# Optimization experiments

Measured on AMD Instinct MI355X. Metric: run time of the kernel, lower is better.

## Reference

```python
import jax, jax.numpy as jnp
import numpy as np

H, W, C = 56, 56, 384
WS, SHIFT, HEADS = 7, 3, 12
HEAD_DIM = C // HEADS
SCALE = HEAD_DIM ** (-0.5)
NWIN = (H // WS) * (W // WS)  # 64 windows per image
NTOK = WS * WS                # 49 tokens per window
EPS = 1e-5


def _gen_mask():
    # static shift-window attention mask, computed with numpy (jit-safe constant)
    img = np.zeros((H, W))
    sl = (slice(0, -WS), slice(-WS, -SHIFT), slice(-SHIFT, None))
    cnt = 0
    for hs in sl:
        for ws in sl:
            img[hs, ws] = cnt
            cnt += 1
    mw = img.reshape(H // WS, WS, W // WS, WS).transpose(0, 2, 1, 3).reshape(-1, NTOK)
    diff = mw[:, None, :] - mw[:, :, None]  # (NWIN, NTOK, NTOK)
    return jnp.asarray(np.where(diff != 0, -100.0, 0.0), dtype=jnp.float32)

ATTN_MASK = _gen_mask()


def _layernorm(x, g, b):
    mu = jnp.mean(x, axis=-1, keepdims=True)
    var = jnp.var(x, axis=-1, keepdims=True)
    return (x - mu) * jax.lax.rsqrt(var + EPS) * g + b


def setup_inputs() -> dict:
    key = jax.random.key(0)
    ks = jax.random.split(key, 6)
    s = 0.02
    return {
        "x": jax.random.normal(ks[0], (16, H * W, C), dtype=jnp.float32),
        "ln1_g": jnp.ones((C,), jnp.float32),
        "ln1_b": jnp.zeros((C,), jnp.float32),
        "qkv_w": jax.random.normal(ks[1], (C, 3 * C), jnp.float32) * s,
        "proj_w": jax.random.normal(ks[2], (C, C), jnp.float32) * s,
        "proj_b": jnp.zeros((C,), jnp.float32),
        "ln2_g": jnp.ones((C,), jnp.float32),
        "ln2_b": jnp.zeros((C,), jnp.float32),
        "fc1_w": jax.random.normal(ks[3], (C, 4 * C), jnp.float32) * s,
        "fc1_b": jnp.zeros((4 * C,), jnp.float32),
        "fc2_w": jax.random.normal(ks[4], (4 * C, C), jnp.float32) * s,
        "fc2_b": jnp.zeros((C,), jnp.float32),
    }


def reference(x, ln1_g, ln1_b, qkv_w, proj_w, proj_b, ln2_g, ln2_b, fc1_w, fc1_b, fc2_w, fc2_b):
    B, N, _ = x.shape
    h = x
    y = _layernorm(x, ln1_g, ln1_b).reshape(B, H, W, C)
    # cyclic shift (note: source never rolls back; we match it)
    y = jnp.roll(y, shift=(-SHIFT, -SHIFT), axis=(1, 2))
    # window partition -> (B*NWIN, NTOK, C)
    y = y.reshape(B, H // WS, WS, W // WS, WS, C).transpose(0, 1, 3, 2, 4, 5)
    y = y.reshape(B * NWIN, NTOK, C)
    # qkv (no bias), split heads
    qkv = (y @ qkv_w).reshape(B * NWIN, NTOK, 3, HEADS, HEAD_DIM)
    qkv = qkv.transpose(2, 0, 3, 1, 4)  # (3, BW, heads, NTOK, hd)
    q, k, v = qkv[0], qkv[1], qkv[2]
    attn = jnp.einsum('whnd,whmd->whnm', q, k) * SCALE  # (BW, heads, NTOK, NTOK)
    attn = attn.reshape(B, NWIN, HEADS, NTOK, NTOK) + ATTN_MASK[None, :, None]
    attn = jax.nn.softmax(attn.reshape(B * NWIN, HEADS, NTOK, NTOK), axis=-1)
    o = jnp.einsum('whnm,whmd->whnd', attn, v)
    o = o.transpose(0, 2, 1, 3).reshape(B * NWIN, NTOK, C)
    o = o @ proj_w + proj_b
    # window reverse -> (B, N, C)
    o = o.reshape(B, H // WS, W // WS, WS, WS, C).transpose(0, 1, 3, 2, 4, 5)
    o = o.reshape(B, N, C)
    x1 = h + o
    # MLP (GELU after both fc1 and fc2, as in source)
    m = _layernorm(x1, ln2_g, ln2_b)
    m = jax.nn.gelu(m @ fc1_w + fc1_b, approximate=False)
    m = jax.nn.gelu(m @ fc2_w + fc2_b, approximate=False)
    return x1 + m
```

## Files before the change

kernel.cpp:

```cpp
#include <hip/hip_runtime.h>
#include <hip/hip_bf16.h>
#include <cstdint>
#include <cstddef>

#define C_DIM   384
#define NIMG    3136
#define MROWS   50176
#define QK_SCALE 0.17677669529663687f

using bf16x8 = __attribute__((ext_vector_type(8))) short;
using f32x4  = __attribute__((ext_vector_type(4))) float;

__device__ __forceinline__ short f2bf(float f) {
  union { float f; uint32_t u; } v; v.f = f;
  uint32_t r = (v.u + 0x7fffu + ((v.u >> 16) & 1u)) >> 16;
  return (short)(uint16_t)r;
}

__device__ __forceinline__ float bf2f(short s) {
  union { uint32_t u; float f; } v; v.u = ((uint32_t)(uint16_t)s) << 16;
  return v.f;
}

__device__ __forceinline__ void async_copy16(const void* g, void* l) {
  __builtin_amdgcn_global_load_lds(
      (const __attribute__((address_space(1))) void*)g,
      (__attribute__((address_space(3))) void*)l, 16, 0, 0);
}

__device__ __forceinline__ float gelu_exact(float x) {
  return 0.5f * x * (1.0f + erff(x * 0.7071067811865475f));
}

__global__ __launch_bounds__(256) void transpose_cast(
    const float* __restrict__ w, short* __restrict__ wt, int K, int N) {
  int idx = blockIdx.x * 256 + threadIdx.x;
  if (idx >= K * N) return;
  int k = idx / N;
  int n = idx - k * N;
  wt[(size_t)n * K + k] = f2bf(w[idx]);
}

template <typename IN>
__global__ __launch_bounds__(256) void ln_kernel(
    const IN* __restrict__ x, const float* __restrict__ g,
    const float* __restrict__ b, short* __restrict__ y, int windowed) {
  int token = blockIdx.x * 4 + (threadIdx.x >> 6);
  int lane = threadIdx.x & 63;
  size_t src;
  if (windowed) {
    int bw = token / 49;
    int tt = token - bw * 49;
    int bb = bw >> 6, w = bw & 63;
    int hs = (w >> 3) * 7 + tt / 7 + 3; if (hs >= 56) hs -= 56;
    int ws = (w & 7) * 7 + (tt % 7) + 3; if (ws >= 56) ws -= 56;
    src = (size_t)(bb * NIMG + hs * 56 + ws) * C_DIM;
  } else {
    src = (size_t)token * C_DIM;
  }
  const IN* xr = x + src;
  float v[6];
  float s = 0.f;
#pragma unroll
  for (int i = 0; i < 6; ++i) {
    if constexpr (sizeof(IN) == 4) v[i] = (float)xr[lane + i * 64];
    else v[i] = bf2f((short)xr[lane + i * 64]);
    s += v[i];
  }
#pragma unroll
  for (int m = 1; m < 64; m <<= 1) s += __shfl_xor(s, m);
  float mu = s * (1.0f / 384.0f);
  float var = 0.f;
#pragma unroll
  for (int i = 0; i < 6; ++i) { float d = v[i] - mu; var += d * d; }
#pragma unroll
  for (int m = 1; m < 64; m <<= 1) var += __shfl_xor(var, m);
  float rstd = rsqrtf(var * (1.0f / 384.0f) + 1e-5f);
  short* yr = y + (size_t)token * C_DIM;
#pragma unroll
  for (int i = 0; i < 6; ++i) {
    int c = lane + i * 64;
    yr[c] = f2bf((v[i] - mu) * rstd * g[c] + b[c]);
  }
}

template <int EPI>
__global__ __launch_bounds__(256, 2) void gemm_kernel(
    const short* __restrict__ A, const short* __restrict__ Bt,
    void* __restrict__ Out, const float* __restrict__ bias,
    const void* __restrict__ resid, int M, int N, int K, int nby) {
  __shared__ __align__(16) short lds[2][128 * 64 * 2];
  const int t = threadIdx.x;
  const int wave = t >> 6, lane = t & 63;
  const int lrow = lane & 15, quad = lane >> 4;
  const int wm = wave & 1, wn = wave >> 1;

  const int wg = (int)blockIdx.x;
  const int swz = (wg & 7) * ((int)gridDim.x >> 3) + (wg >> 3);
  const int mb = swz / nby;
  const int nb = swz - mb * nby;
  const int m0 = mb * 128, n0 = nb * 128;

  f32x4 acc[4][4] = {};

  const int srow = t >> 3;
  const int spos = t & 7;

  const int nt = K >> 6;

  auto stage = [&](int buf, int k0) {
    short* la = &lds[buf][0];
    short* lb = la + 128 * 64;
#pragma unroll
    for (int i = 0; i < 4; ++i) {
      int row = i * 32 + srow;
      int ca = spos ^ (row & 7);
      async_copy16(A + (size_t)(m0 + row) * K + k0 + ca * 8,
                   la + (i * 32 + wave * 8) * 64);
      async_copy16(Bt + (size_t)(n0 + row) * K + k0 + ca * 8,
                   lb + (i * 32 + wave * 8) * 64);
    }
  };

  stage(0, 0);

  for (int kt = 0; kt < nt; ++kt) {
    __builtin_amdgcn_sched_barrier(0);
    if (kt + 1 < nt) {
      stage((kt + 1) & 1, (kt + 1) * 64);
      asm volatile("s_waitcnt vmcnt(8)" ::: "memory");
    } else {
      asm volatile("s_waitcnt vmcnt(0)" ::: "memory");
    }
    __builtin_amdgcn_s_barrier();
    __builtin_amdgcn_sched_barrier(0);

    short* ldsA = &lds[kt & 1][0];
    short* ldsB = ldsA + 128 * 64;
#pragma unroll
    for (int ks = 0; ks < 2; ++ks) {
      const int cb = ks * 4;
      bf16x8 af[4], bfr[4];
#pragma unroll
      for (int i = 0; i < 4; ++i) {
        int ra = wm * 64 + i * 16 + lrow;
        af[i] = *(const bf16x8*)(ldsA + ra * 64 + (((cb + quad) ^ (ra & 7)) * 8));
        int rb = wn * 64 + i * 16 + lrow;
        bfr[i] = *(const bf16x8*)(ldsB + rb * 64 + (((cb + quad) ^ (rb & 7)) * 8));
      }
      __builtin_amdgcn_s_setprio(1);
#pragma unroll
      for (int i = 0; i < 4; ++i)
#pragma unroll
        for (int j = 0; j < 4; ++j)
          acc[i][j] = __builtin_amdgcn_mfma_f32_16x16x32_bf16(af[i], bfr[j],
                                                              acc[i][j], 0, 0, 0);
      __builtin_amdgcn_s_setprio(0);
    }
    __builtin_amdgcn_sched_barrier(0);
    __builtin_amdgcn_s_barrier();
  }

#pragma unroll
  for (int i = 0; i < 4; ++i) {
#pragma unroll
    for (int r = 0; r < 4; ++r) {
      int row = m0 + wm * 64 + i * 16 + quad * 4 + r;
      if (EPI == 1) {
        int bw = row / 49;
        int tt = row - bw * 49;
        int bb = bw >> 6, w = bw & 63;
        int nimg = ((w >> 3) * 7 + tt / 7) * 56 + (w & 7) * 7 + (tt % 7);
        size_t obase = ((size_t)(bb * NIMG + nimg)) * C_DIM;
#pragma unroll
        for (int j = 0; j < 4; ++j) {
          int col = n0 + wn * 64 + j * 16 + lrow;
          size_t oi = obase + col;
          ((short*)Out)[oi] =
              f2bf(acc[i][j][r] + bias[col] + ((const float*)resid)[oi]);
        }
      } else {
#pragma unroll
        for (int j = 0; j < 4; ++j) {
          int col = n0 + wn * 64 + j * 16 + lrow;
          float v = acc[i][j][r];
          if (EPI == 0) {
            ((short*)Out)[(size_t)row * N + col] = f2bf(v);
          } else if (EPI == 2) {
            ((short*)Out)[(size_t)row * N + col] = f2bf(gelu_exact(v + bias[col]));
          } else {
            size_t oi = (size_t)row * C_DIM + col;
            ((float*)Out)[oi] =
                bf2f(((const short*)resid)[oi]) + gelu_exact(v + bias[col]);
          }
        }
      }
    }
  }
}

__global__ __launch_bounds__(256) void attn_kernel(
    const short* __restrict__ qkv, short* __restrict__ o) {
  __shared__ __align__(16) short plds[4][64 * 72];
  const int wavei = threadIdx.x >> 6;
  const int lane = threadIdx.x & 63;
  const int gw = blockIdx.x * 4 + wavei;
  const int bw = gw / 12;
  const int h = gw - bw * 12;
  const int w = bw & 63;
  const int lrow = lane & 15, quad = lane >> 4;
  const short* base = qkv + (size_t)bw * 49 * 1152 + h * 32;

  bf16x8 qf[4], kf[4];
#pragma unroll
  for (int i = 0; i < 4; ++i) {
    int tq = i * 16 + lrow;
    const short* p = base + (size_t)tq * 1152 + quad * 8;
    qf[i] = *(const bf16x8*)p;
    kf[i] = *(const bf16x8*)(p + 384);
  }
  f32x4 sa[4][4] = {};
#pragma unroll
  for (int i = 0; i < 4; ++i)
#pragma unroll
    for (int j = 0; j < 4; ++j)
      sa[i][j] = __builtin_amdgcn_mfma_f32_16x16x32_bf16(qf[i], kf[j], sa[i][j], 0, 0, 0);

  int tl = lane < 49 ? lane : 0;
  int rr = tl / 7, cc = tl - rr * 7;
  int hs = (w >> 3) * 7 + rr;
  int ws = (w & 7) * 7 + cc;
  int id = (hs < 49 ? 0 : (hs < 53 ? 3 : 6)) + (ws < 49 ? 0 : (ws < 53 ? 1 : 2));

  int idn[4], idm[4][4];
#pragma unroll
  for (int j = 0; j < 4; ++j) idn[j] = __shfl(id, j * 16 + lrow);
#pragma unroll
  for (int i = 0; i < 4; ++i)
#pragma unroll
    for (int r = 0; r < 4; ++r) idm[i][r] = __shfl(id, i * 16 + quad * 4 + r);

#pragma unroll
  for (int i = 0; i < 4; ++i)
#pragma unroll
    for (int j = 0; j < 4; ++j)
#pragma unroll
      for (int r = 0; r < 4; ++r) {
        float v = sa[i][j][r] * QK_SCALE + (idm[i][r] == idn[j] ? 0.f : -100.f);
        sa[i][j][r] = (j * 16 + lrow < 49) ? v : -1e30f;
      }

#pragma unroll
  for (int i = 0; i < 4; ++i)
#pragma unroll
    for (int r = 0; r < 4; ++r) {
      float mx = -1e30f;
#pragma unroll
      for (int j = 0; j < 4; ++j) mx = fmaxf(mx, sa[i][j][r]);
#pragma unroll
      for (int m = 1; m < 16; m <<= 1) mx = fmaxf(mx, __shfl_xor(mx, m));
      float sum = 0.f;
#pragma unroll
      for (int j = 0; j < 4; ++j) {
        float e = exp2f((sa[i][j][r] - mx) * 1.44269504f);
        sa[i][j][r] = e;
        sum += e;
      }
#pragma unroll
      for (int m = 1; m < 16; m <<= 1) sum += __shfl_xor(sum, m);
      float inv = 1.0f / sum;
#pragma unroll
      for (int j = 0; j < 4; ++j) sa[i][j][r] *= inv;
    }

  short* pw = plds[wavei];
#pragma unroll
  for (int i = 0; i < 4; ++i)
#pragma unroll
    for (int r = 0; r < 4; ++r)
#pragma unroll
      for (int j = 0; j < 4; ++j)
        pw[(i * 16 + quad * 4 + r) * 72 + j * 16 + lrow] = f2bf(sa[i][j][r]);

  f32x4 oa[4][2] = {};
#pragma unroll
  for (int kk = 0; kk < 2; ++kk) {
    bf16x8 vf[2];
#pragma unroll
    for (int j2 = 0; j2 < 2; ++j2) {
#pragma unroll
      for (int jj = 0; jj < 8; ++jj) {
        int n = kk * 32 + quad * 8 + jj;
        vf[j2][jj] = (n < 49)
            ? base[768 + (size_t)n * 1152 + j2 * 16 + lrow]
            : (short)0;
      }
    }
#pragma unroll
    for (int i = 0; i < 4; ++i) {
      bf16x8 pf = *(const bf16x8*)(pw + (i * 16 + lrow) * 72 + kk * 32 + quad * 8);
#pragma unroll
      for (int j2 = 0; j2 < 2; ++j2)
        oa[i][j2] = __builtin_amdgcn_mfma_f32_16x16x32_bf16(pf, vf[j2], oa[i][j2], 0, 0, 0);
    }
  }

#pragma unroll
  for (int i = 0; i < 4; ++i)
#pragma unroll
    for (int j2 = 0; j2 < 2; ++j2)
#pragma unroll
      for (int r = 0; r < 4; ++r) {
        int m = i * 16 + quad * 4 + r;
        if (m < 49)
          o[((size_t)bw * 49 + m) * 384 + h * 32 + j2 * 16 + lrow] = f2bf(oa[i][j2][r]);
      }
}

extern "C" void kernel_launch(void* const* d_in, const int* in_sizes, int n_in,
                              void* d_out, int out_size, void* d_ws, size_t ws_size,
                              hipStream_t stream) {
  const float* x      = (const float*)d_in[0];
  const float* ln1_g  = (const float*)d_in[1];
  const float* ln1_b  = (const float*)d_in[2];
  const float* qkv_w  = (const float*)d_in[3];
  const float* proj_w = (const float*)d_in[4];
  const float* proj_b = (const float*)d_in[5];
  const float* ln2_g  = (const float*)d_in[6];
  const float* ln2_b  = (const float*)d_in[7];
  const float* fc1_w  = (const float*)d_in[8];
  const float* fc1_b  = (const float*)d_in[9];
  const float* fc2_w  = (const float*)d_in[10];
  const float* fc2_b  = (const float*)d_in[11];
  float* out = (float*)d_out;

  char* ws = (char*)d_ws;
  auto alloc = [&](size_t bytes) {
    char* p = ws;
    ws += (bytes + 255) & ~(size_t)255;
    return p;
  };
  short* qkv_wT  = (short*)alloc((size_t)1152 * 384 * 2);
  short* proj_wT = (short*)alloc((size_t)384 * 384 * 2);
  short* fc1_wT  = (short*)alloc((size_t)1536 * 384 * 2);
  short* fc2_wT  = (short*)alloc((size_t)384 * 1536 * 2);
  short* bufA    = (short*)alloc((size_t)MROWS * 384 * 2);
  short* x1      = (short*)alloc((size_t)MROWS * 384 * 2);
  short* bufB    = (short*)alloc((size_t)MROWS * 1536 * 2);

  transpose_cast<<<(384 * 1152) / 256, 256, 0, stream>>>(qkv_w, qkv_wT, 384, 1152);
  transpose_cast<<<(384 * 384) / 256, 256, 0, stream>>>(proj_w, proj_wT, 384, 384);
  transpose_cast<<<(384 * 1536) / 256, 256, 0, stream>>>(fc1_w, fc1_wT, 384, 1536);
  transpose_cast<<<(1536 * 384) / 256, 256, 0, stream>>>(fc2_w, fc2_wT, 1536, 384);

  ln_kernel<float><<<MROWS / 4, 256, 0, stream>>>(x, ln1_g, ln1_b, bufA, 1);

  gemm_kernel<0><<<392 * 9, 256, 0, stream>>>(bufA, qkv_wT, bufB, nullptr,
                                              nullptr, MROWS, 1152, 384, 9);

  attn_kernel<<<3072, 256, 0, stream>>>(bufB, bufA);

  gemm_kernel<1><<<392 * 3, 256, 0, stream>>>(bufA, proj_wT, x1, proj_b,
                                              x, MROWS, 384, 384, 3);

  ln_kernel<short><<<MROWS / 4, 256, 0, stream>>>(x1, ln2_g, ln2_b, bufA, 0);

  gemm_kernel<2><<<392 * 12, 256, 0, stream>>>(bufA, fc1_wT, bufB, fc1_b,
                                               nullptr, MROWS, 1536, 384, 12);

  gemm_kernel<3><<<392 * 3, 256, 0, stream>>>(bufB, fc2_wT, out, fc2_b,
                                              x1, MROWS, 384, 1536, 3);
}
```

Measured before the change: 572.7 us.

## Add single-buffer high-occupancy GEMM variant for short-K GEMMs and fast GELU

Adds a PIPE template parameter to the GEMM. The K=384 GEMMs (qkv, proj, fc1) now use a single LDS buffer with plain syncthreads staging and launch bounds allowing 4 blocks per CU. Only the K=1536 fc2 GEMM keeps the double-buffered pipeline. The erf-based GELU is also replaced by an Abramowitz-Stegun polynomial with a hardware reciprocal and exp2, which cuts epilogue cost but is slightly less accurate.

```diff
diff --git a/kernel.cpp b/kernel.cpp
--- a/kernel.cpp
+++ b/kernel.cpp
@@ -28,8 +28,15 @@
       (__attribute__((address_space(3))) void*)l, 16, 0, 0);
 }
 
-__device__ __forceinline__ float gelu_exact(float x) {
-  return 0.5f * x * (1.0f + erff(x * 0.7071067811865475f));
+__device__ __forceinline__ float gelu_fast(float x) {
+  float z = fabsf(x) * 0.7071067811865476f;
+  float t = __builtin_amdgcn_rcpf(fmaf(0.3275911f, z, 1.0f));
+  float p = t * fmaf(t, fmaf(t, fmaf(t, fmaf(t, 1.061405429f, -1.453152027f),
+                                     1.421413741f), -0.284496736f),
+                     0.254829592f);
+  float e = p * exp2f(z * z * -1.4426950408889634f);
+  float phi2 = (x >= 0.0f) ? (2.0f - e) : e;
+  return 0.5f * x * phi2;
 }
 
 __global__ __launch_bounds__(256) void transpose_cast(
@@ -84,12 +91,13 @@
   }
 }
 
-template <int EPI>
-__global__ __launch_bounds__(256, 2) void gemm_kernel(
+template <int EPI, int PIPE>
+__global__ __launch_bounds__(256, PIPE ? 2 : 4) void gemm_kernel(
     const short* __restrict__ A, const short* __restrict__ Bt,
     void* __restrict__ Out, const float* __restrict__ bias,
     const void* __restrict__ resid, int M, int N, int K, int nby) {
-  __shared__ __align__(16) short lds[2][128 * 64 * 2];
+  constexpr int NBUF = PIPE ? 2 : 1;
+  __shared__ __align__(16) short lds[NBUF][128 * 64 * 2];
   const int t = threadIdx.x;
   const int wave = t >> 6, lane = t & 63;
   const int lrow = lane & 15, quad = lane >> 4;
@@ -122,20 +130,8 @@
     }
   };
 
-  stage(0, 0);
-
-  for (int kt = 0; kt < nt; ++kt) {
-    __builtin_amdgcn_sched_barrier(0);
-    if (kt + 1 < nt) {
-      stage((kt + 1) & 1, (kt + 1) * 64);
-      asm volatile("s_waitcnt vmcnt(8)" ::: "memory");
-    } else {
-      asm volatile("s_waitcnt vmcnt(0)" ::: "memory");
-    }
-    __builtin_amdgcn_s_barrier();
-    __builtin_amdgcn_sched_barrier(0);
-
-    short* ldsA = &lds[kt & 1][0];
+  auto compute = [&](int buf) {
+    short* ldsA = &lds[buf][0];
     short* ldsB = ldsA + 128 * 64;
 #pragma unroll
     for (int ks = 0; ks < 2; ++ks) {
@@ -148,17 +144,40 @@
         int rb = wn * 64 + i * 16 + lrow;
         bfr[i] = *(const bf16x8*)(ldsB + rb * 64 + (((cb + quad) ^ (rb & 7)) * 8));
       }
-      __builtin_amdgcn_s_setprio(1);
+      if (PIPE) __builtin_amdgcn_s_setprio(1);
 #pragma unroll
       for (int i = 0; i < 4; ++i)
 #pragma unroll
         for (int j = 0; j < 4; ++j)
           acc[i][j] = __builtin_amdgcn_mfma_f32_16x16x32_bf16(af[i], bfr[j],
                                                               acc[i][j], 0, 0, 0);
-      __builtin_amdgcn_s_setprio(0);
-    }
-    __builtin_amdgcn_sched_barrier(0);
-    __builtin_amdgcn_s_barrier();
+      if (PIPE) __builtin_amdgcn_s_setprio(0);
+    }
+  };
+
+  if constexpr (PIPE == 0) {
+    for (int kt = 0; kt < nt; ++kt) {
+      __syncthreads();
+      stage(0, kt * 64);
+      __syncthreads();
+      compute(0);
+    }
+  } else {
+    stage(0, 0);
+    for (int kt = 0; kt < nt; ++kt) {
+      __builtin_amdgcn_sched_barrier(0);
+      if (kt + 1 < nt) {
+        stage((kt + 1) & 1, (kt + 1) * 64);
+        asm volatile("s_waitcnt vmcnt(8)" ::: "memory");
+      } else {
+        asm volatile("s_waitcnt vmcnt(0)" ::: "memory");
+      }
+      __builtin_amdgcn_s_barrier();
+      __builtin_amdgcn_sched_barrier(0);
+      compute(kt & 1);
+      __builtin_amdgcn_sched_barrier(0);
+      __builtin_amdgcn_s_barrier();
+    }
   }
 
 #pragma unroll
@@ -187,11 +206,11 @@
           if (EPI == 0) {
             ((short*)Out)[(size_t)row * N + col] = f2bf(v);
           } else if (EPI == 2) {
-            ((short*)Out)[(size_t)row * N + col] = f2bf(gelu_exact(v + bias[col]));
+            ((short*)Out)[(size_t)row * N + col] = f2bf(gelu_fast(v + bias[col]));
           } else {
             size_t oi = (size_t)row * C_DIM + col;
             ((float*)Out)[oi] =
-                bf2f(((const short*)resid)[oi]) + gelu_exact(v + bias[col]);
+                bf2f(((const short*)resid)[oi]) + gelu_fast(v + bias[col]);
           }
         }
       }
@@ -355,19 +374,19 @@
 
   ln_kernel<float><<<MROWS / 4, 256, 0, stream>>>(x, ln1_g, ln1_b, bufA, 1);
 
-  gemm_kernel<0><<<392 * 9, 256, 0, stream>>>(bufA, qkv_wT, bufB, nullptr,
-                                              nullptr, MROWS, 1152, 384, 9);
+  gemm_kernel<0, 0><<<392 * 9, 256, 0, stream>>>(bufA, qkv_wT, bufB, nullptr,
+                                                 nullptr, MROWS, 1152, 384, 9);
 
   attn_kernel<<<3072, 256, 0, stream>>>(bufB, bufA);
 
-  gemm_kernel<1><<<392 * 3, 256, 0, stream>>>(bufA, proj_wT, x1, proj_b,
-                                              x, MROWS, 384, 384, 3);
+  gemm_kernel<1, 0><<<392 * 3, 256, 0, stream>>>(bufA, proj_wT, x1, proj_b,
+                                                 x, MROWS, 384, 384, 3);
 
   ln_kernel<short><<<MROWS / 4, 256, 0, stream>>>(x1, ln2_g, ln2_b, bufA, 0);
 
-  gemm_kernel<2><<<392 * 12, 256, 0, stream>>>(bufA, fc1_wT, bufB, fc1_b,
-                                               nullptr, MROWS, 1536, 384, 12);
-
-  gemm_kernel<3><<<392 * 3, 256, 0, stream>>>(bufB, fc2_wT, out, fc2_b,
-                                              x1, MROWS, 384, 1536, 3);
-}
+  gemm_kernel<2, 0><<<392 * 12, 256, 0, stream>>>(bufA, fc1_wT, bufB, fc1_b,
+                                                  nullptr, MROWS, 1536, 384, 12);
+
+  gemm_kernel<3, 1><<<392 * 3, 256, 0, stream>>>(bufB, fc2_wT, out, fc2_b,
+                                                 x1, MROWS, 384, 1536, 3);
+}
```

Result: faster. 525.8 us (-8.2%).
